# Optimization experiments

Measured on AMD Instinct MI355X. Metric: run time of the kernel, lower is better.

## Reference

```python
import jax, jax.numpy as jnp
import numpy as np

EPS_BN = 1e-5   # torch BatchNorm1d default eps
EPS_D = 1e-8    # pointops interpolation eps
K = 3           # pointops.nearestneighbor returns 3 nearest neighbors

B, N1, N2 = 4, 8192, 2048
IN_PLANES, OUT_PLANES = 512, 256


def setup_inputs() -> dict:
    key = jax.random.key(0)
    ks = jax.random.split(key, 8)
    return {
        "p1": jax.random.normal(ks[0], (B, N1, 3), jnp.float32),
        "x1": jax.random.normal(ks[1], (B, N1, OUT_PLANES), jnp.float32),
        "p2": jax.random.normal(ks[2], (B, N2, 3), jnp.float32),
        "x2": jax.random.normal(ks[3], (B, N2, IN_PLANES), jnp.float32),
        # linear1: Linear(out_planes, out_planes) + BN + ReLU (acts on x1)
        "W1": jax.random.normal(ks[4], (OUT_PLANES, OUT_PLANES), jnp.float32) / np.sqrt(OUT_PLANES),
        "b1": jax.random.normal(ks[5], (OUT_PLANES,), jnp.float32) * 0.01,
        "gamma1": jnp.ones((OUT_PLANES,), jnp.float32),
        "beta1": jnp.zeros((OUT_PLANES,), jnp.float32),
        # linear2: Linear(in_planes, out_planes) + BN + ReLU (acts on x2)
        "W2": jax.random.normal(ks[6], (IN_PLANES, OUT_PLANES), jnp.float32) / np.sqrt(IN_PLANES),
        "b2": jax.random.normal(ks[7], (OUT_PLANES,), jnp.float32) * 0.01,
        "gamma2": jnp.ones((OUT_PLANES,), jnp.float32),
        "beta2": jnp.zeros((OUT_PLANES,), jnp.float32),
    }


def _bn(x, gamma, beta):
    # BatchNorm1d_P: normalize each channel over (batch, points) with batch stats
    m = jnp.mean(x, axis=(0, 1))
    v = jnp.var(x, axis=(0, 1))
    return (x - m) * jax.lax.rsqrt(v + EPS_BN) * gamma + beta


def reference(p1, x1, p2, x2, W1, b1, gamma1, beta1, W2, b2, gamma2, beta2):
    # linear2 on coarse features: [B,N2,in] -> [B,N2,out]
    h2 = jax.nn.relu(_bn(x2 @ W2 + b2, gamma2, beta2))
    # 3-NN of each p1 point among p2 points, squared distances [B,N1,N2]
    d = (jnp.sum(p1 * p1, -1)[:, :, None]
         + jnp.sum(p2 * p2, -1)[:, None, :]
         - 2.0 * jnp.einsum('bnd,bmd->bnm', p1, p2))
    neg_d, idx = jax.lax.top_k(-d, K)          # [B,N1,K]
    dist = -neg_d
    dist_recip = 1.0 / (dist + EPS_D)
    weight = dist_recip / jnp.sum(dist_recip, -1, keepdims=True)  # [B,N1,K]
    gathered = jax.vmap(lambda f, i: f[i])(h2, idx)               # [B,N1,K,out]
    interp = jnp.einsum('bnk,bnkc->bnc', weight, gathered)        # [B,N1,out]
    # linear1 on fine features: [B,N1,out] -> [B,N1,out]
    h1 = jax.nn.relu(_bn(x1 @ W1 + b1, gamma1, beta1))
    return interp + h1
```

## Files before the change

### kernel.cpp

```cpp
#include <hip/hip_runtime.h>
#include <stdint.h>

#define B_   4
#define N1_  8192
#define N2_  2048
#define CIN  512
#define COUT 256

typedef __attribute__((ext_vector_type(8))) short bf16x8;
typedef __attribute__((ext_vector_type(4))) float f32x4;

__device__ inline short f2bf(float f) {
  union { float f; unsigned u; } v; v.f = f;
  unsigned r = v.u + 0x7fffu + ((v.u >> 16) & 1u);
  return (short)(r >> 16);
}
__device__ inline float bf2f(short s) {
  union { unsigned u; float f; } v; v.u = ((unsigned)(unsigned short)s) << 16;
  return v.f;
}
__device__ inline float relu_(float x) { return fmaxf(x, 0.0f); }

#define INS3(d, j, d0, d1, d2, i0, i1, i2)                                \
  { bool lt0 = (d) < d0, lt1 = (d) < d1, lt2 = (d) < d2;                  \
    d2 = lt1 ? d1 : (lt2 ? (d) : d2); i2 = lt1 ? i1 : (lt2 ? (j) : i2);   \
    d1 = lt0 ? d0 : (lt1 ? (d) : d1); i1 = lt0 ? i0 : (lt1 ? (j) : i1);   \
    d0 = lt0 ? (d) : d0;              i0 = lt0 ? (j) : i0; }

typedef const __attribute__((address_space(1))) unsigned int* gas_t;
typedef __attribute__((address_space(3))) unsigned int* las_t;
__device__ __forceinline__ void g2l16(const short* g, short* l) {
  __builtin_amdgcn_global_load_lds((gas_t)g, (las_t)l, 16, 0, 0);
}

#define KNN_B  256
#define CV1_B0 256
#define CV2_B0 8448
#define W1_B0  12544
#define W2_B0  12800
#define ST_B0  13312
#define TOT_B  13316

__global__ __launch_bounds__(256) void knn_prep(
    const float* __restrict__ p1, const float* __restrict__ p2,
    const float* __restrict__ W1, const float* __restrict__ W2,
    const float* __restrict__ x1, const float* __restrict__ x2,
    float* __restrict__ wgt, int* __restrict__ idx,
    short* __restrict__ Wt1, short* __restrict__ Wt2,
    short* __restrict__ x1b, short* __restrict__ x2b,
    float* __restrict__ stats)
{
  __shared__ float4 sp2[N2_];
  const int bid = blockIdx.x;
  const int tid = threadIdx.x;

  if (bid >= KNN_B) {
    if (bid < CV2_B0) {
      int i = (bid - CV1_B0) * 256 + tid;
      float4 v = ((const float4*)x1)[i];
      short4 s = { f2bf(v.x), f2bf(v.y), f2bf(v.z), f2bf(v.w) };
      ((short4*)x1b)[i] = s;
    } else if (bid < W1_B0) {
      int i = (bid - CV2_B0) * 256 + tid;
      float4 v = ((const float4*)x2)[i];
      short4 s = { f2bf(v.x), f2bf(v.y), f2bf(v.z), f2bf(v.w) };
      ((short4*)x2b)[i] = s;
    } else if (bid < W2_B0) {
      int k = (bid - W1_B0) * 256 + tid;
      Wt1[(size_t)(k & 255) * COUT + (k >> 8)] = f2bf(W1[k]);
    } else if (bid < ST_B0) {
      int k = (bid - W2_B0) * 256 + tid;
      Wt2[(size_t)(k & 255) * CIN + (k >> 8)] = f2bf(W2[k]);
    } else {
      stats[(bid - ST_B0) * 256 + tid] = 0.0f;
    }
    return;
  }

  const int b = bid & 3;
  const int qg = bid >> 2;
  const float* P2 = p2 + (size_t)b * N2_ * 3;
  for (int j = tid; j < N2_; j += 256) {
    float x = P2[j * 3 + 0], y = P2[j * 3 + 1], z = P2[j * 3 + 2];
    sp2[j] = make_float4(x, y, z, x * x + y * y + z * z);
  }
  __syncthreads();

  const int sub = tid & 7;
  const int g = tid >> 3;
  float nx[4], ny[4], nz[4], s1[4];
  #pragma unroll
  for (int qi = 0; qi < 4; qi++) {
    const int q = qg * 128 + qi * 32 + g;
    const float* P1 = p1 + ((size_t)b * N1_ + q) * 3;
    float x = P1[0], y = P1[1], z = P1[2];
    s1[qi] = x * x + y * y + z * z;
    nx[qi] = -2.0f * x; ny[qi] = -2.0f * y; nz[qi] = -2.0f * z;
  }
  float t0[4], t1[4], t2[4];
  int i0[4], i1[4], i2[4];
  #pragma unroll
  for (int qi = 0; qi < 4; qi++) {
    t0[qi] = 1e30f; t1[qi] = 1e30f; t2[qi] = 1e30f;
    i0[qi] = 0; i1[qi] = 0; i2[qi] = 0;
  }

  const float4* base = &sp2[sub];
  int jb = sub;
  for (int t = 0; t < 32; t++) {
    #pragma unroll
    for (int u = 0; u < 8; u++) {
      float4 qq = base[u * 8];
      const int jv = jb + u * 8;
      #pragma unroll
      for (int qi = 0; qi < 4; qi++) {
        float d = fmaf(nx[qi], qq.x, fmaf(ny[qi], qq.y, fmaf(nz[qi], qq.z, qq.w)));
        INS3(d, jv, t0[qi], t1[qi], t2[qi], i0[qi], i1[qi], i2[qi]);
      }
    }
    base += 64;
    jb += 64;
  }

  #pragma unroll
  for (int m = 1; m < 8; m <<= 1) {
    #pragma unroll
    for (int qi = 0; qi < 4; qi++) {
      float e0 = __shfl_xor(t0[qi], m);
      float e1 = __shfl_xor(t1[qi], m);
      float e2 = __shfl_xor(t2[qi], m);
      int j0 = __shfl_xor(i0[qi], m);
      int j1 = __shfl_xor(i1[qi], m);
      int j2 = __shfl_xor(i2[qi], m);
      INS3(e0, j0, t0[qi], t1[qi], t2[qi], i0[qi], i1[qi], i2[qi]);
      INS3(e1, j1, t0[qi], t1[qi], t2[qi], i0[qi], i1[qi], i2[qi]);
      INS3(e2, j2, t0[qi], t1[qi], t2[qi], i0[qi], i1[qi], i2[qi]);
    }
  }

  if (sub == 0) {
    #pragma unroll
    for (int qi = 0; qi < 4; qi++) {
      const int q = qg * 128 + qi * 32 + g;
      float r0 = 1.0f / (t0[qi] + s1[qi] + 1e-8f);
      float r1 = 1.0f / (t1[qi] + s1[qi] + 1e-8f);
      float r2 = 1.0f / (t2[qi] + s1[qi] + 1e-8f);
      float rs = 1.0f / (r0 + r1 + r2);
      size_t o = ((size_t)b * N1_ + q) * 3;
      wgt[o + 0] = r0 * rs; wgt[o + 1] = r1 * rs; wgt[o + 2] = r2 * rs;
      idx[o + 0] = i0[qi];  idx[o + 1] = i1[qi];  idx[o + 2] = i2[qi];
    }
  }
}

#define GBM 128
#define GBN 128
#define GBK 64

__global__ __launch_bounds__(256) void gemm_fused(
    const short* __restrict__ x1b, const short* __restrict__ x2b,
    const short* __restrict__ Wt1, const short* __restrict__ Wt2,
    const float* __restrict__ bias1, const float* __restrict__ bias2,
    short* __restrict__ y1, short* __restrict__ y2,
    float* __restrict__ stats)
{
  __shared__ __align__(16) short As[GBM * GBK];
  __shared__ __align__(16) short Bs[GBN * GBK];

  const int bid = blockIdx.x;
  const short* X; const short* Wt; const float* bias; short* Y; float* st;
  int K, mb, nb;
  if (bid < 128) {
    X = x2b; Wt = Wt2; bias = bias2; Y = y2; st = stats + 512; K = CIN;
    mb = bid >> 1; nb = bid & 1;
  } else {
    const int t = bid - 128;
    X = x1b; Wt = Wt1; bias = bias1; Y = y1; st = stats; K = COUT;
    mb = t >> 1; nb = t & 1;
  }
  const int bm = mb * GBM;
  const int bn = nb * GBN;

  const int tid = threadIdx.x, lane = tid & 63, wave = tid >> 6;
  const int wm = (wave & 1) * 64, wn = (wave >> 1) * 64;

  f32x4 acc[4][4];
  #pragma unroll
  for (int i = 0; i < 4; i++)
    #pragma unroll
    for (int j = 0; j < 4; j++)
      #pragma unroll
      for (int e = 0; e < 4; e++) acc[i][j][e] = 0.0f;

  const int lr = lane >> 3;
  const int lp = (lane & 7) ^ lr;
  const int lk = lp * 8;

  const int fr = lane & 15;
  const int quad = lane >> 4;
  const int pA0 = ((quad ^ (fr & 7)) * 16);

  for (int k0 = 0; k0 < K; k0 += GBK) {
    #pragma unroll
    for (int i = 0; i < 4; i++) {
      const int crow = wave * 4 + i;
      g2l16(X  + (size_t)(bm + crow * 8 + lr) * K + k0 + lk, As + crow * 512);
      g2l16(Wt + (size_t)(bn + crow * 8 + lr) * K + k0 + lk, Bs + crow * 512);
    }
    __syncthreads();

    #pragma unroll
    for (int ks = 0; ks < 2; ks++) {
      const int xo = ks * 64;
      bf16x8 af[4], bfr[4];
      #pragma unroll
      for (int i = 0; i < 4; i++) {
        af[i]  = *(const bf16x8*)((const char*)As + (wm + i * 16 + fr) * 128 + (pA0 ^ xo));
        bfr[i] = *(const bf16x8*)((const char*)Bs + (wn + i * 16 + fr) * 128 + (pA0 ^ xo));
      }
      #pragma unroll
      for (int i = 0; i < 4; i++)
        #pragma unroll
        for (int j = 0; j < 4; j++)
          acc[i][j] = __builtin_amdgcn_mfma_f32_16x16x32_bf16(af[i], bfr[j], acc[i][j], 0, 0, 0);
    }
    __syncthreads();
  }

  const int col = fr;
  const int rq = quad * 4;
  float cs[4], cs2[4];
  #pragma unroll
  for (int ni = 0; ni < 4; ni++) { cs[ni] = 0.0f; cs2[ni] = 0.0f; }

  #pragma unroll
  for (int mi = 0; mi < 4; mi++) {
    #pragma unroll
    for (int ni = 0; ni < 4; ni++) {
      const int gm = bm + wm + mi * 16 + rq;
      const int gn = bn + wn + ni * 16 + col;
      const float bb = bias[gn];
      #pragma unroll
      for (int j = 0; j < 4; j++) {
        float v = acc[mi][ni][j] + bb;
        Y[(size_t)(gm + j) * 256 + gn] = f2bf(v);
        cs[ni] += v;
        cs2[ni] += v * v;
      }
    }
  }
  #pragma unroll
  for (int ni = 0; ni < 4; ni++) {
    cs[ni]  += __shfl_xor(cs[ni], 16);  cs[ni]  += __shfl_xor(cs[ni], 32);
    cs2[ni] += __shfl_xor(cs2[ni], 16); cs2[ni] += __shfl_xor(cs2[ni], 32);
  }
  if (lane < 16) {
    #pragma unroll
    for (int ni = 0; ni < 4; ni++) {
      const int gn = bn + wn + ni * 16 + col;
      atomicAdd(&st[gn], cs[ni]);
      atomicAdd(&st[256 + gn], cs2[ni]);
    }
  }
}

__global__ __launch_bounds__(256) void final_out(
    const short* __restrict__ y1, const short* __restrict__ y2,
    const float* __restrict__ stats,
    const float* __restrict__ gamma1, const float* __restrict__ beta1,
    const float* __restrict__ gamma2, const float* __restrict__ beta2,
    const float* __restrict__ wgt, const int* __restrict__ idx,
    float* __restrict__ out)
{
  const int r = blockIdx.x * 4 + (threadIdx.x >> 6);
  const int lane = threadIdx.x & 63;
  const int b = r >> 13;
  const int c = lane * 4;

  const float invM1 = 1.0f / (B_ * N1_), invM2 = 1.0f / (B_ * N2_);
  float4 su1 = *(const float4*)&stats[c];
  float4 sq1 = *(const float4*)&stats[256 + c];
  float4 su2 = *(const float4*)&stats[512 + c];
  float4 sq2 = *(const float4*)&stats[768 + c];
  float4 gm1 = *(const float4*)&gamma1[c];
  float4 bt1 = *(const float4*)&beta1[c];
  float4 gm2 = *(const float4*)&gamma2[c];
  float4 bt2 = *(const float4*)&beta2[c];

  float4 sc1, sh1, sc2, sh2;
  {
    float m, v;
    m = su1.x * invM1; v = sq1.x * invM1 - m * m; sc1.x = gm1.x * rsqrtf(v + 1e-5f); sh1.x = bt1.x - m * sc1.x;
    m = su1.y * invM1; v = sq1.y * invM1 - m * m; sc1.y = gm1.y * rsqrtf(v + 1e-5f); sh1.y = bt1.y - m * sc1.y;
    m = su1.z * invM1; v = sq1.z * invM1 - m * m; sc1.z = gm1.z * rsqrtf(v + 1e-5f); sh1.z = bt1.z - m * sc1.z;
    m = su1.w * invM1; v = sq1.w * invM1 - m * m; sc1.w = gm1.w * rsqrtf(v + 1e-5f); sh1.w = bt1.w - m * sc1.w;
    m = su2.x * invM2; v = sq2.x * invM2 - m * m; sc2.x = gm2.x * rsqrtf(v + 1e-5f); sh2.x = bt2.x - m * sc2.x;
    m = su2.y * invM2; v = sq2.y * invM2 - m * m; sc2.y = gm2.y * rsqrtf(v + 1e-5f); sh2.y = bt2.y - m * sc2.y;
    m = su2.z * invM2; v = sq2.z * invM2 - m * m; sc2.z = gm2.z * rsqrtf(v + 1e-5f); sh2.z = bt2.z - m * sc2.z;
    m = su2.w * invM2; v = sq2.w * invM2 - m * m; sc2.w = gm2.w * rsqrtf(v + 1e-5f); sh2.w = bt2.w - m * sc2.w;
  }

  const size_t wo = (size_t)r * 3;
  const float w0 = wgt[wo], w1 = wgt[wo + 1], w2 = wgt[wo + 2];
  const int i0 = idx[wo], i1 = idx[wo + 1], i2 = idx[wo + 2];

  const short* g0 = y2 + ((size_t)b * N2_ + i0) * 256;
  const short* g1 = y2 + ((size_t)b * N2_ + i1) * 256;
  const short* g2 = y2 + ((size_t)b * N2_ + i2) * 256;

  short4 s0 = *(const short4*)&g0[c];
  short4 s1 = *(const short4*)&g1[c];
  short4 s2 = *(const short4*)&g2[c];
  short4 sv = *(const short4*)&y1[(size_t)r * 256 + c];

  float4 o;
  o.x = w0 * relu_(bf2f(s0.x) * sc2.x + sh2.x) + w1 * relu_(bf2f(s1.x) * sc2.x + sh2.x)
      + w2 * relu_(bf2f(s2.x) * sc2.x + sh2.x) + relu_(bf2f(sv.x) * sc1.x + sh1.x);
  o.y = w0 * relu_(bf2f(s0.y) * sc2.y + sh2.y) + w1 * relu_(bf2f(s1.y) * sc2.y + sh2.y)
      + w2 * relu_(bf2f(s2.y) * sc2.y + sh2.y) + relu_(bf2f(sv.y) * sc1.y + sh1.y);
  o.z = w0 * relu_(bf2f(s0.z) * sc2.z + sh2.z) + w1 * relu_(bf2f(s1.z) * sc2.z + sh2.z)
      + w2 * relu_(bf2f(s2.z) * sc2.z + sh2.z) + relu_(bf2f(sv.z) * sc1.z + sh1.z);
  o.w = w0 * relu_(bf2f(s0.w) * sc2.w + sh2.w) + w1 * relu_(bf2f(s1.w) * sc2.w + sh2.w)
      + w2 * relu_(bf2f(s2.w) * sc2.w + sh2.w) + relu_(bf2f(sv.w) * sc1.w + sh1.w);

  *(float4*)&out[(size_t)r * 256 + c] = o;
}

extern "C" void kernel_launch(void* const* d_in, const int* in_sizes, int n_in,
                              void* d_out, int out_size, void* d_ws, size_t ws_size,
                              hipStream_t stream)
{
  const float* p1  = (const float*)d_in[0];
  const float* x1  = (const float*)d_in[1];
  const float* p2  = (const float*)d_in[2];
  const float* x2  = (const float*)d_in[3];
  const float* W1  = (const float*)d_in[4];
  const float* b1  = (const float*)d_in[5];
  const float* g1  = (const float*)d_in[6];
  const float* be1 = (const float*)d_in[7];
  const float* W2  = (const float*)d_in[8];
  const float* b2  = (const float*)d_in[9];
  const float* g2  = (const float*)d_in[10];
  const float* be2 = (const float*)d_in[11];
  float* out = (float*)d_out;
  char* ws = (char*)d_ws;

  short* y1    = (short*)(ws + 0);
  short* y2    = (short*)(ws + 16777216);
  short* x1b   = (short*)(ws + 20971520);
  short* x2b   = (short*)(ws + 37748736);
  short* Wt1   = (short*)(ws + 46137344);
  short* Wt2   = (short*)(ws + 46268416);
  float* stats = (float*)(ws + 46530560);
  float* wgt   = (float*)(ws + 46534656);
  int*   idx   = (int*)  (ws + 46927872);

  knn_prep<<<TOT_B, 256, 0, stream>>>(p1, p2, W1, W2, x1, x2,
                                      wgt, idx, Wt1, Wt2, x1b, x2b, stats);

  gemm_fused<<<640, 256, 0, stream>>>(x1b, x2b, Wt1, Wt2, b1, b2, y1, y2, stats);

  final_out<<<(B_ * N1_) / 4, 256, 0, stream>>>(
      y1, y2, stats, g1, be1, g2, be2, wgt, idx, out);
}
```

Before: 191.1 us.

## Split KNN search across 32 lanes per query and batch conversion blocks

The KNN phase now spreads each query's scan of the 2048 candidate points over 32 lanes instead of 8, and each block handles 32 queries instead of 128, so the KNN grid grows from 256 to 1024 blocks and fills the GPU better. Each lane scans fewer candidates but the shuffle merge of top-3 lists grows from 3 to 5 rounds. Each block also recomputes the shared p2 table, so 1024 blocks now repeat that staging work. The conversion, weight-transpose and stats-zeroing blocks each do 4 elements per thread, cutting their block count roughly fourfold.

Result: faster. 183.4 us (-4.0%).

```diff
diff --git a/kernel.cpp b/kernel.cpp
--- a/kernel.cpp
+++ b/kernel.cpp
@@ -33,13 +33,13 @@
   __builtin_amdgcn_global_load_lds((gas_t)g, (las_t)l, 16, 0, 0);
 }
 
-#define KNN_B  256
-#define CV1_B0 256
-#define CV2_B0 8448
-#define W1_B0  12544
-#define W2_B0  12800
-#define ST_B0  13312
-#define TOT_B  13316
+#define KNN_B  1024
+#define CV1_B0 1024
+#define CV2_B0 3072
+#define W1_B0  4096
+#define W2_B0  4160
+#define ST_B0  4288
+#define TOT_B  4289
 
 __global__ __launch_bounds__(256) void knn_prep(
     const float* __restrict__ p1, const float* __restrict__ p2,
@@ -56,23 +56,40 @@
 
   if (bid >= KNN_B) {
     if (bid < CV2_B0) {
-      int i = (bid - CV1_B0) * 256 + tid;
-      float4 v = ((const float4*)x1)[i];
-      short4 s = { f2bf(v.x), f2bf(v.y), f2bf(v.z), f2bf(v.w) };
-      ((short4*)x1b)[i] = s;
+      int i0_ = (bid - CV1_B0) * 1024 + tid;
+      #pragma unroll
+      for (int r = 0; r < 4; r++) {
+        int i = i0_ + r * 256;
+        float4 v = ((const float4*)x1)[i];
+        short4 s = { f2bf(v.x), f2bf(v.y), f2bf(v.z), f2bf(v.w) };
+        ((short4*)x1b)[i] = s;
+      }
     } else if (bid < W1_B0) {
-      int i = (bid - CV2_B0) * 256 + tid;
-      float4 v = ((const float4*)x2)[i];
-      short4 s = { f2bf(v.x), f2bf(v.y), f2bf(v.z), f2bf(v.w) };
-      ((short4*)x2b)[i] = s;
+      int i0_ = (bid - CV2_B0) * 1024 + tid;
+      #pragma unroll
+      for (int r = 0; r < 4; r++) {
+        int i = i0_ + r * 256;
+        float4 v = ((const float4*)x2)[i];
+        short4 s = { f2bf(v.x), f2bf(v.y), f2bf(v.z), f2bf(v.w) };
+        ((short4*)x2b)[i] = s;
+      }
     } else if (bid < W2_B0) {
-      int k = (bid - W1_B0) * 256 + tid;
-      Wt1[(size_t)(k & 255) * COUT + (k >> 8)] = f2bf(W1[k]);
+      int k0_ = (bid - W1_B0) * 1024 + tid;
+      #pragma unroll
+      for (int r = 0; r < 4; r++) {
+        int k = k0_ + r * 256;
+        Wt1[(size_t)(k & 255) * COUT + (k >> 8)] = f2bf(W1[k]);
+      }
     } else if (bid < ST_B0) {
-      int k = (bid - W2_B0) * 256 + tid;
-      Wt2[(size_t)(k & 255) * CIN + (k >> 8)] = f2bf(W2[k]);
+      int k0_ = (bid - W2_B0) * 1024 + tid;
+      #pragma unroll
+      for (int r = 0; r < 4; r++) {
+        int k = k0_ + r * 256;
+        Wt2[(size_t)(k & 255) * CIN + (k >> 8)] = f2bf(W2[k]);
+      }
     } else {
-      stats[(bid - ST_B0) * 256 + tid] = 0.0f;
+      #pragma unroll
+      for (int r = 0; r < 4; r++) stats[r * 256 + tid] = 0.0f;
     }
     return;
   }
@@ -86,12 +103,12 @@
   }
   __syncthreads();
 
-  const int sub = tid & 7;
-  const int g = tid >> 3;
+  const int sub = tid & 31;
+  const int g32 = tid >> 5;
   float nx[4], ny[4], nz[4], s1[4];
   #pragma unroll
   for (int qi = 0; qi < 4; qi++) {
-    const int q = qg * 128 + qi * 32 + g;
+    const int q = qg * 32 + qi * 8 + g32;
     const float* P1 = p1 + ((size_t)b * N1_ + q) * 3;
     float x = P1[0], y = P1[1], z = P1[2];
     s1[qi] = x * x + y * y + z * z;
@@ -107,23 +124,23 @@
 
   const float4* base = &sp2[sub];
   int jb = sub;
-  for (int t = 0; t < 32; t++) {
+  for (int t = 0; t < 8; t++) {
     #pragma unroll
     for (int u = 0; u < 8; u++) {
-      float4 qq = base[u * 8];
-      const int jv = jb + u * 8;
+      float4 qq = base[u * 32];
+      const int jv = jb + u * 32;
       #pragma unroll
       for (int qi = 0; qi < 4; qi++) {
         float d = fmaf(nx[qi], qq.x, fmaf(ny[qi], qq.y, fmaf(nz[qi], qq.z, qq.w)));
         INS3(d, jv, t0[qi], t1[qi], t2[qi], i0[qi], i1[qi], i2[qi]);
       }
     }
-    base += 64;
-    jb += 64;
-  }
-
-  #pragma unroll
-  for (int m = 1; m < 8; m <<= 1) {
+    base += 256;
+    jb += 256;
+  }
+
+  #pragma unroll
+  for (int m = 1; m < 32; m <<= 1) {
     #pragma unroll
     for (int qi = 0; qi < 4; qi++) {
       float e0 = __shfl_xor(t0[qi], m);
@@ -141,7 +158,7 @@
   if (sub == 0) {
     #pragma unroll
     for (int qi = 0; qi < 4; qi++) {
-      const int q = qg * 128 + qi * 32 + g;
+      const int q = qg * 32 + qi * 8 + g32;
       float r0 = 1.0f / (t0[qi] + s1[qi] + 1e-8f);
       float r1 = 1.0f / (t1[qi] + s1[qi] + 1e-8f);
       float r2 = 1.0f / (t2[qi] + s1[qi] + 1e-8f);
```
